# Kernel optimization log

Hardware: AMD Instinct MI355X
Metric: run time of the kernel (lower is better)

## Reference

```python
import jax, jax.numpy as jnp
import numpy as np

D_MODEL = 1024
NUM_HEADS = 16
HEAD_DIM = D_MODEL // NUM_HEADS
ALPHA = 1.0


def setup_inputs() -> dict:
    key = jax.random.key(0)
    ks = jax.random.split(key, 9)
    B, T, D = 2, 2048, D_MODEL
    s = 1.0 / np.sqrt(D)
    inp = {
        "x": jax.random.normal(ks[0], (B, T, D), dtype=jnp.float32),
        "Wq": jax.random.uniform(ks[1], (D, D), jnp.float32, -s, s),
        "bq": jax.random.uniform(ks[2], (D,), jnp.float32, -s, s),
        "Wk": jax.random.uniform(ks[3], (D, D), jnp.float32, -s, s),
        "bk": jax.random.uniform(ks[4], (D,), jnp.float32, -s, s),
        "Wv": jax.random.uniform(ks[5], (D, D), jnp.float32, -s, s),
        "bv": jax.random.uniform(ks[6], (D,), jnp.float32, -s, s),
        "Wo": jax.random.uniform(ks[7], (D, D), jnp.float32, -s, s),
        "bo": jax.random.uniform(ks[8], (D,), jnp.float32, -s, s),
    }
    return inp


def reference(x, Wq, bq, Wk, bk, Wv, bv, Wo, bo):
    B, T, D = x.shape
    H, hd = NUM_HEADS, HEAD_DIM

    def split_heads(y):  # [B,T,D] -> [B,H,T,hd]
        return y.reshape(B, T, H, hd).transpose(0, 2, 1, 3)

    Q = split_heads(x @ Wq.T + bq)
    K = split_heads(x @ Wk.T + bk)
    V = split_heads(x @ Wv.T + bv)

    scores = jnp.einsum('bhid,bhjd->bhij', Q, K) / jnp.sqrt(jnp.float32(hd))

    t = jnp.arange(T)
    delta = t[:, None] - t[None, :]  # [T,T], i - j
    causal_mask = delta < 0          # j > i (strict upper triangle)
    # similarity_power_law decay bias: -(delta)^alpha for delta >= 0, else 0
    decay = jnp.where(causal_mask, 0.0, -(delta.astype(jnp.float32) ** ALPHA))

    scores = jnp.where(causal_mask, -jnp.inf, scores) + decay
    attn = jax.nn.softmax(scores, axis=-1)

    out = jnp.einsum('bhij,bhjd->bhid', attn, V)
    out = out.transpose(0, 2, 1, 3).reshape(B, T, D)
    return out @ Wo.T + bo
```

## Files before the change

### kernel.cpp

```cpp
#include <hip/hip_runtime.h>

#define TT 2048
#define DD 1024
#define HH 16
#define HD 64
#define NTOK 4096
#define BK 32

typedef __bf16 bf16x8 __attribute__((ext_vector_type(8)));
typedef short short4v __attribute__((ext_vector_type(4)));
typedef float f32x4 __attribute__((ext_vector_type(4)));

__device__ __forceinline__ unsigned short f2bf(float f) {
  unsigned u = __float_as_uint(f);
  u += 0x7fffu + ((u >> 16) & 1u);
  return (unsigned short)(u >> 16);
}

#if __has_builtin(__builtin_amdgcn_mfma_f32_16x16x16bf16_1k)
__device__ __forceinline__ f32x4 mfma16(short4v a, short4v b, f32x4 c) {
  return __builtin_amdgcn_mfma_f32_16x16x16bf16_1k(a, b, c, 0, 0, 0);
}
#else
__device__ __forceinline__ f32x4 mfma16(short4v a, short4v b, f32x4 c) {
  asm("v_mfma_f32_16x16x16_bf16 %0, %1, %2, %0\n\ts_nop 7\n\ts_nop 7"
      : "+v"(c) : "v"(a), "v"(b));
  return c;
}
#endif

typedef void __attribute__((address_space(1))) as1_void;
typedef void __attribute__((address_space(3))) as3_void;
__device__ __forceinline__ void gl_lds16(const void* g, void* l) {
  __builtin_amdgcn_global_load_lds((as1_void*)g, (as3_void*)l, 16, 0, 0);
}

__global__ __launch_bounds__(256)
void wcmha_cast_all(const float4* __restrict__ x,  const float4* __restrict__ wq,
                    const float4* __restrict__ wk, const float4* __restrict__ wv,
                    const float4* __restrict__ wo,
                    ushort4* __restrict__ xb,  ushort4* __restrict__ wqb,
                    ushort4* __restrict__ wkb, ushort4* __restrict__ wvb,
                    ushort4* __restrict__ wob) {
  const int i = blockIdx.x * 256 + threadIdx.x;
  const float4* src;
  ushort4* dst;
  int off;
  if (i < 1048576) {
    src = x; dst = xb; off = i;
  } else {
    int j = i - 1048576;
    int sel = j >> 18;
    off = j & 262143;
    const float4* ws_[4] = {wq, wk, wv, wo};
    ushort4* wd_[4] = {wqb, wkb, wvb, wob};
    src = ws_[sel]; dst = wd_[sel];
  }
  float4 v = src[off];
  ushort4 o;
  o.x = f2bf(v.x); o.y = f2bf(v.y); o.z = f2bf(v.z); o.w = f2bf(v.w);
  dst[off] = o;
}

template <bool SWAP>
__device__ __forceinline__ void gemm128_core(
    const unsigned short* __restrict__ X, const unsigned short* __restrict__ W,
    int m0, int n0, unsigned short* As, unsigned short* Bs, f32x4 acc[4][4]) {
  const int tid = threadIdx.x;
  const int wid = tid >> 6, lane = tid & 63;
  const int m = lane & 15, quad = lane >> 4;
  const int wm = (wid >> 1) * 64, wn = (wid & 1) * 64;

  const int c0 = wid * 64 + lane;
  const int c1 = c0 + 256;
  const unsigned short* ga0 = X + (size_t)(m0 + (c0 >> 2)) * DD + (c0 & 3) * 8;
  const unsigned short* ga1 = X + (size_t)(m0 + (c1 >> 2)) * DD + (c1 & 3) * 8;
  const unsigned short* gb0 = W + (size_t)(n0 + (c0 >> 2)) * DD + (c0 & 3) * 8;
  const unsigned short* gb1 = W + (size_t)(n0 + (c1 >> 2)) * DD + (c1 & 3) * 8;
  unsigned short* la0 = As + wid * 512;
  unsigned short* la1 = As + 2048 + wid * 512;
  unsigned short* lb0 = Bs + wid * 512;
  unsigned short* lb1 = Bs + 2048 + wid * 512;

#pragma unroll
  for (int i = 0; i < 4; ++i)
#pragma unroll
    for (int j = 0; j < 4; ++j) acc[i][j] = (f32x4){0.f, 0.f, 0.f, 0.f};

  for (int k0 = 0; k0 < DD; k0 += BK) {
    gl_lds16(ga0 + k0, la0);
    gl_lds16(ga1 + k0, la1);
    gl_lds16(gb0 + k0, lb0);
    gl_lds16(gb1 + k0, lb1);
    __syncthreads();
    bf16x8 af[4], bf[4];
#pragma unroll
    for (int mi = 0; mi < 4; ++mi)
      af[mi] = *(const bf16x8*)&As[(wm + mi * 16 + m) * BK + quad * 8];
#pragma unroll
    for (int ni = 0; ni < 4; ++ni)
      bf[ni] = *(const bf16x8*)&Bs[(wn + ni * 16 + m) * BK + quad * 8];
#pragma unroll
    for (int mi = 0; mi < 4; ++mi)
#pragma unroll
      for (int ni = 0; ni < 4; ++ni)
        acc[mi][ni] = SWAP
            ? __builtin_amdgcn_mfma_f32_16x16x32_bf16(bf[ni], af[mi], acc[mi][ni], 0, 0, 0)
            : __builtin_amdgcn_mfma_f32_16x16x32_bf16(af[mi], bf[ni], acc[mi][ni], 0, 0, 0);
    __syncthreads();
  }
}

__global__ __launch_bounds__(256)
void wcmha_gemm_qkv(const unsigned short* __restrict__ X,
                    const unsigned short* __restrict__ Wq,
                    const unsigned short* __restrict__ Wk,
                    const unsigned short* __restrict__ Wv,
                    const float* __restrict__ bq, const float* __restrict__ bk,
                    const float* __restrict__ bv,
                    unsigned short* __restrict__ Qb,
                    unsigned short* __restrict__ Kb,
                    unsigned short* __restrict__ Vt) {
  __shared__ unsigned short As[128 * BK];
  __shared__ unsigned short Bs[128 * BK];
  const int mat = blockIdx.y >> 3;
  const int m0 = blockIdx.x * 128;
  const int n0 = (blockIdx.y & 7) * 128;

  const int lane = threadIdx.x & 63, wid = threadIdx.x >> 6;
  const int m = lane & 15, quad = lane >> 4;
  const int wm = (wid >> 1) * 64, wn = (wid & 1) * 64;

  f32x4 acc[4][4];
  if (mat < 2) {
    const unsigned short* W = mat ? Wk : Wq;
    const float* bias = mat ? bk : bq;
    unsigned short* dst = mat ? Kb : Qb;
    gemm128_core<false>(X, W, m0, n0, As, Bs, acc);
#pragma unroll
    for (int mi = 0; mi < 4; ++mi)
#pragma unroll
      for (int ni = 0; ni < 4; ++ni) {
        int col = n0 + wn + ni * 16 + m;
        int h = col >> 6, d = col & 63;
        float bb = bias[col];
#pragma unroll
        for (int r = 0; r < 4; ++r) {
          int row = m0 + wm + mi * 16 + quad * 4 + r;
          int b = row >> 11, t = row & (TT - 1);
          dst[((size_t)(b * HH + h) * TT + t) * HD + d] = f2bf(acc[mi][ni][r] + bb);
        }
      }
  } else {
    gemm128_core<true>(X, Wv, m0, n0, As, Bs, acc);
#pragma unroll
    for (int mi = 0; mi < 4; ++mi) {
      int row = m0 + wm + mi * 16 + m;
      int b = row >> 11, t = row & (TT - 1);
#pragma unroll
      for (int ni = 0; ni < 4; ++ni)
#pragma unroll
        for (int r = 0; r < 4; ++r) {
          int col = n0 + wn + ni * 16 + quad * 4 + r;
          int h = col >> 6, d = col & 63;
          Vt[((size_t)(b * HH + h) * HD + d) * TT + t] = f2bf(acc[mi][ni][r] + bv[col]);
        }
    }
  }
}

__global__ __launch_bounds__(256)
void wcmha_gemm_out(const unsigned short* __restrict__ X,
                    const unsigned short* __restrict__ W,
                    const float* __restrict__ bias,
                    float* __restrict__ Y) {
  __shared__ unsigned short As[128 * BK];
  __shared__ unsigned short Bs[64 * BK];
  const int tid = threadIdx.x;
  const int wid = tid >> 6, lane = tid & 63;
  const int m = lane & 15, quad = lane >> 4;
  const int m0 = blockIdx.x * 128;
  const int n0 = blockIdx.y * 64;
  const int wm = (wid >> 1) * 64, wn = (wid & 1) * 32;

  const int ca0 = wid * 128 + lane;
  const int ca1 = ca0 + 64;
  const int cb  = wid * 64 + lane;
  const unsigned short* aga = X + (size_t)(m0 + (ca0 >> 2)) * DD + (ca0 & 3) * 8;
  const unsigned short* agb = X + (size_t)(m0 + (ca1 >> 2)) * DD + (ca1 & 3) * 8;
  const unsigned short* bga = W + (size_t)(n0 + (cb >> 2)) * DD + (cb & 3) * 8;
  unsigned short* lda = &As[wid * 1024];
  unsigned short* ldb = &As[wid * 1024 + 512];
  unsigned short* ldc = &Bs[wid * 512];

  f32x4 acc[4][2];
#pragma unroll
  for (int i = 0; i < 4; ++i)
#pragma unroll
    for (int j = 0; j < 2; ++j) acc[i][j] = (f32x4){0.f, 0.f, 0.f, 0.f};

  for (int k0 = 0; k0 < DD; k0 += BK) {
    gl_lds16(aga + k0, lda);
    gl_lds16(agb + k0, ldb);
    gl_lds16(bga + k0, ldc);
    __syncthreads();
    bf16x8 af[4], bf[2];
#pragma unroll
    for (int mi = 0; mi < 4; ++mi)
      af[mi] = *(const bf16x8*)&As[(wm + mi * 16 + m) * BK + quad * 8];
#pragma unroll
    for (int ni = 0; ni < 2; ++ni)
      bf[ni] = *(const bf16x8*)&Bs[(wn + ni * 16 + m) * BK + quad * 8];
#pragma unroll
    for (int mi = 0; mi < 4; ++mi)
#pragma unroll
      for (int ni = 0; ni < 2; ++ni)
        acc[mi][ni] = __builtin_amdgcn_mfma_f32_16x16x32_bf16(af[mi], bf[ni], acc[mi][ni], 0, 0, 0);
    __syncthreads();
  }

#pragma unroll
  for (int mi = 0; mi < 4; ++mi)
#pragma unroll
    for (int ni = 0; ni < 2; ++ni) {
      int col = n0 + wn + ni * 16 + m;
      float bb = bias[col];
#pragma unroll
      for (int r = 0; r < 4; ++r) {
        int row = m0 + wm + mi * 16 + quad * 4 + r;
        Y[(size_t)row * DD + col] = acc[mi][ni][r] + bb;
      }
    }
}

__global__ __launch_bounds__(256)
void wcmha_attn(const unsigned short* __restrict__ Qb,
                const unsigned short* __restrict__ Kb,
                const unsigned short* __restrict__ Vt,
                unsigned short* __restrict__ O) {
  const int wid = threadIdx.x >> 6, lane = threadIdx.x & 63;
  const int gw = (blockIdx.x << 2) + wid;
  const int qt = gw & 127, bh = gw >> 7;
  const int qbase = qt << 4;
  const int il = lane & 15, quad = lane >> 4;
  const int ig = qbase + il;

  const unsigned short* q_ptr = Qb + (size_t)bh * TT * HD;
  const unsigned short* k_ptr = Kb + (size_t)bh * TT * HD;
  const unsigned short* v_ptr = Vt + (size_t)bh * HD * TT;

  const bf16x8 qf0 = *(const bf16x8*)(q_ptr + (size_t)ig * HD + quad * 8);
  const bf16x8 qf1 = *(const bf16x8*)(q_ptr + (size_t)ig * HD + 32 + quad * 8);

  const int j0 = (qbase >= 48) ? qbase - 48 : 0;

  f32x4 st[4];
#pragma unroll
  for (int jt = 0; jt < 4; ++jt) {
    const unsigned short* kp = k_ptr + (size_t)(j0 + jt * 16 + il) * HD;
    bf16x8 k0 = *(const bf16x8*)(kp + quad * 8);
    bf16x8 k1 = *(const bf16x8*)(kp + 32 + quad * 8);
    f32x4 a = {0.f, 0.f, 0.f, 0.f};
    a = __builtin_amdgcn_mfma_f32_16x16x32_bf16(k0, qf0, a, 0, 0, 0);
    a = __builtin_amdgcn_mfma_f32_16x16x32_bf16(k1, qf1, a, 0, 0, 0);
    st[jt] = a;
  }

  float mloc = -3.0e38f;
#pragma unroll
  for (int jt = 0; jt < 4; ++jt)
#pragma unroll
    for (int r = 0; r < 4; ++r) {
      int jg = j0 + jt * 16 + quad * 4 + r;
      float v = (jg > ig) ? -3.0e38f : st[jt][r] * 0.125f - (float)(ig - jg);
      st[jt][r] = v;
      mloc = fmaxf(mloc, v);
    }
  mloc = fmaxf(mloc, __shfl_xor(mloc, 16));
  mloc = fmaxf(mloc, __shfl_xor(mloc, 32));

  float rs = 0.f;
  short4v pf[4];
#pragma unroll
  for (int jt = 0; jt < 4; ++jt)
#pragma unroll
    for (int r = 0; r < 4; ++r) {
      float p = __expf(st[jt][r] - mloc);
      rs += p;
      pf[jt][r] = (short)f2bf(p);
    }
  rs += __shfl_xor(rs, 16);
  rs += __shfl_xor(rs, 32);

  f32x4 o_acc[4];
#pragma unroll
  for (int nt = 0; nt < 4; ++nt) o_acc[nt] = (f32x4){0.f, 0.f, 0.f, 0.f};
#pragma unroll
  for (int jt = 0; jt < 4; ++jt)
#pragma unroll
    for (int nt = 0; nt < 4; ++nt) {
      short4v vf = *(const short4v*)(v_ptr + (size_t)(nt * 16 + il) * TT +
                                     j0 + jt * 16 + quad * 4);
      o_acc[nt] = mfma16(vf, pf[jt], o_acc[nt]);
    }

  const float inv_l = 1.f / rs;
  const int b = bh >> 4, hh = bh & 15;
  unsigned short* ob = O + ((size_t)(b * TT + ig)) * DD + hh * HD;
#pragma unroll
  for (int nt = 0; nt < 4; ++nt)
#pragma unroll
    for (int r = 0; r < 4; ++r)
      ob[nt * 16 + quad * 4 + r] = f2bf(o_acc[nt][r] * inv_l);
}

extern "C" void kernel_launch(void* const* d_in, const int* in_sizes, int n_in,
                              void* d_out, int out_size, void* d_ws, size_t ws_size,
                              hipStream_t stream) {
  const float* x  = (const float*)d_in[0];
  const float* Wq = (const float*)d_in[1];
  const float* bq = (const float*)d_in[2];
  const float* Wk = (const float*)d_in[3];
  const float* bk = (const float*)d_in[4];
  const float* Wv = (const float*)d_in[5];
  const float* bv = (const float*)d_in[6];
  const float* Wo = (const float*)d_in[7];
  const float* bo = (const float*)d_in[8];

  char* ws = (char*)d_ws;
  unsigned short* xb  = (unsigned short*)(ws);
  unsigned short* wqb = (unsigned short*)(ws + (8u << 20));
  unsigned short* wkb = wqb + (1u << 20);
  unsigned short* wvb = wkb + (1u << 20);
  unsigned short* wob = wvb + (1u << 20);
  unsigned short* Qb  = (unsigned short*)(ws + (16u << 20));
  unsigned short* Kb  = (unsigned short*)(ws + (24u << 20));
  unsigned short* Vt  = (unsigned short*)(ws + (32u << 20));
  unsigned short* Ob  = xb;

  wcmha_cast_all<<<8192, 256, 0, stream>>>(
      (const float4*)x, (const float4*)Wq, (const float4*)Wk,
      (const float4*)Wv, (const float4*)Wo,
      (ushort4*)xb, (ushort4*)wqb, (ushort4*)wkb, (ushort4*)wvb, (ushort4*)wob);

  wcmha_gemm_qkv<<<dim3(32, 24), 256, 0, stream>>>(xb, wqb, wkb, wvb,
                                                   bq, bk, bv, Qb, Kb, Vt);

  wcmha_attn<<<1024, 256, 0, stream>>>(Qb, Kb, Vt, Ob);

  wcmha_gemm_out<<<dim3(32, 16), 256, 0, stream>>>(Ob, wob, bo, (float*)d_out);
}
```

Baseline: 170.0 us.

## Double-buffer GEMM LDS tiles with XOR swizzle and unify QKV/out GEMM core

Replaces the single-buffered GEMM main loop with a double-buffered one. The next K tile's global-to-LDS loads are issued before the current tile is computed, and one barrier per iteration replaces two. Each row's 16-byte chunk index is XOR-swizzled on both the load and the read side to reduce LDS bank conflicts. Both the QKV and output projection kernels now share a templated core, at the cost of twice the LDS per block, which may lower occupancy.

```diff
diff --git a/kernel.cpp b/kernel.cpp
--- a/kernel.cpp
+++ b/kernel.cpp
@@ -5,7 +5,6 @@
 #define HH 16
 #define HD 64
 #define NTOK 4096
-#define BK 32
 
 typedef __bf16 bf16x8 __attribute__((ext_vector_type(8)));
 typedef short short4v __attribute__((ext_vector_type(4)));
@@ -62,52 +61,79 @@
   dst[off] = o;
 }
 
-template <bool SWAP>
-__device__ __forceinline__ void gemm128_core(
-    const unsigned short* __restrict__ X, const unsigned short* __restrict__ W,
-    int m0, int n0, unsigned short* As, unsigned short* Bs, f32x4 acc[4][4]) {
-  const int tid = threadIdx.x;
-  const int wid = tid >> 6, lane = tid & 63;
+template <int BN_, bool SWAP>
+__device__ __forceinline__ void gemm_db(const unsigned short* __restrict__ X,
+                                        const unsigned short* __restrict__ W,
+                                        int m0, int n0,
+                                        unsigned short* As, unsigned short* Bs,
+                                        f32x4 acc[4][BN_ / 32]) {
+  constexpr int NI = BN_ / 32;
+  constexpr int JB = (BN_ * 4) / 256;
+  const int tid = threadIdx.x, wid = tid >> 6, lane = tid & 63;
   const int m = lane & 15, quad = lane >> 4;
-  const int wm = (wid >> 1) * 64, wn = (wid & 1) * 64;
-
-  const int c0 = wid * 64 + lane;
-  const int c1 = c0 + 256;
-  const unsigned short* ga0 = X + (size_t)(m0 + (c0 >> 2)) * DD + (c0 & 3) * 8;
-  const unsigned short* ga1 = X + (size_t)(m0 + (c1 >> 2)) * DD + (c1 & 3) * 8;
-  const unsigned short* gb0 = W + (size_t)(n0 + (c0 >> 2)) * DD + (c0 & 3) * 8;
-  const unsigned short* gb1 = W + (size_t)(n0 + (c1 >> 2)) * DD + (c1 & 3) * 8;
-  unsigned short* la0 = As + wid * 512;
-  unsigned short* la1 = As + 2048 + wid * 512;
-  unsigned short* lb0 = Bs + wid * 512;
-  unsigned short* lb1 = Bs + 2048 + wid * 512;
+  const int wm = (wid >> 1) * 64, wn = (wid & 1) * (BN_ / 2);
+  const int xq = (quad ^ ((m >> 1) & 3)) * 8;
+
+  const unsigned short* gA[2];
+  const unsigned short* gB[JB];
+#pragma unroll
+  for (int j = 0; j < 2; ++j) {
+    int c = wid * 64 + lane + j * 256;
+    gA[j] = X + (size_t)(m0 + (c >> 2)) * DD + ((c & 3) ^ ((c >> 3) & 3)) * 8;
+  }
+#pragma unroll
+  for (int j = 0; j < JB; ++j) {
+    int c = wid * 64 + lane + j * 256;
+    gB[j] = W + (size_t)(n0 + (c >> 2)) * DD + ((c & 3) ^ ((c >> 3) & 3)) * 8;
+  }
+  unsigned short* lA[2][2];
+  unsigned short* lB[2][JB];
+#pragma unroll
+  for (int p = 0; p < 2; ++p) {
+#pragma unroll
+    for (int j = 0; j < 2; ++j)
+      lA[p][j] = As + p * (128 * 32) + (wid * 64 + j * 256) * 8;
+#pragma unroll
+    for (int j = 0; j < JB; ++j)
+      lB[p][j] = Bs + p * (BN_ * 32) + (wid * 64 + j * 256) * 8;
+  }
 
 #pragma unroll
   for (int i = 0; i < 4; ++i)
 #pragma unroll
-    for (int j = 0; j < 4; ++j) acc[i][j] = (f32x4){0.f, 0.f, 0.f, 0.f};
-
-  for (int k0 = 0; k0 < DD; k0 += BK) {
-    gl_lds16(ga0 + k0, la0);
-    gl_lds16(ga1 + k0, la1);
-    gl_lds16(gb0 + k0, lb0);
-    gl_lds16(gb1 + k0, lb1);
+    for (int j = 0; j < NI; ++j) acc[i][j] = (f32x4){0.f, 0.f, 0.f, 0.f};
+
+#pragma unroll
+  for (int j = 0; j < 2; ++j) gl_lds16(gA[j], lA[0][j]);
+#pragma unroll
+  for (int j = 0; j < JB; ++j) gl_lds16(gB[j], lB[0][j]);
+
+  for (int k = 0; k < 32; ++k) {
+    const int p = k & 1;
     __syncthreads();
-    bf16x8 af[4], bf[4];
+    if (k < 31) {
+      const int k1 = (k + 1) * 32;
+#pragma unroll
+      for (int j = 0; j < 2; ++j) gl_lds16(gA[j] + k1, lA[p ^ 1][j]);
+#pragma unroll
+      for (int j = 0; j < JB; ++j) gl_lds16(gB[j] + k1, lB[p ^ 1][j]);
+    }
+    const unsigned short* ap = As + p * (128 * 32);
+    const unsigned short* bp = Bs + p * (BN_ * 32);
+    bf16x8 af[4], bf[NI];
 #pragma unroll
     for (int mi = 0; mi < 4; ++mi)
-      af[mi] = *(const bf16x8*)&As[(wm + mi * 16 + m) * BK + quad * 8];
-#pragma unroll
-    for (int ni = 0; ni < 4; ++ni)
-      bf[ni] = *(const bf16x8*)&Bs[(wn + ni * 16 + m) * BK + quad * 8];
+      af[mi] = *(const bf16x8*)&ap[(wm + mi * 16 + m) * 32 + xq];
+#pragma unroll
+    for (int ni = 0; ni < NI; ++ni)
+      bf[ni] = *(const bf16x8*)&bp[(wn + ni * 16 + m) * 32 + xq];
 #pragma unroll
     for (int mi = 0; mi < 4; ++mi)
 #pragma unroll
-      for (int ni = 0; ni < 4; ++ni)
+      for (int ni = 0; ni < NI; ++ni)
         acc[mi][ni] = SWAP
             ? __builtin_amdgcn_mfma_f32_16x16x32_bf16(bf[ni], af[mi], acc[mi][ni], 0, 0, 0)
             : __builtin_amdgcn_mfma_f32_16x16x32_bf16(af[mi], bf[ni], acc[mi][ni], 0, 0, 0);
-    __syncthreads();
   }
 }
 
@@ -121,8 +147,8 @@
                     unsigned short* __restrict__ Qb,
                     unsigned short* __restrict__ Kb,
                     unsigned short* __restrict__ Vt) {
-  __shared__ unsigned short As[128 * BK];
-  __shared__ unsigned short Bs[128 * BK];
+  __shared__ unsigned short As[2 * 128 * 32];
+  __shared__ unsigned short Bs[2 * 128 * 32];
   const int mat = blockIdx.y >> 3;
   const int m0 = blockIdx.x * 128;
   const int n0 = (blockIdx.y & 7) * 128;
@@ -136,7 +162,7 @@
     const unsigned short* W = mat ? Wk : Wq;
     const float* bias = mat ? bk : bq;
     unsigned short* dst = mat ? Kb : Qb;
-    gemm128_core<false>(X, W, m0, n0, As, Bs, acc);
+    gemm_db<128, false>(X, W, m0, n0, As, Bs, acc);
 #pragma unroll
     for (int mi = 0; mi < 4; ++mi)
 #pragma unroll
@@ -152,7 +178,7 @@
         }
       }
   } else {
-    gemm128_core<true>(X, Wv, m0, n0, As, Bs, acc);
+    gemm_db<128, true>(X, Wv, m0, n0, As, Bs, acc);
 #pragma unroll
     for (int mi = 0; mi < 4; ++mi) {
       int row = m0 + wm + mi * 16 + m;
@@ -174,50 +200,16 @@
                     const unsigned short* __restrict__ W,
                     const float* __restrict__ bias,
                     float* __restrict__ Y) {
-  __shared__ unsigned short As[128 * BK];
-  __shared__ unsigned short Bs[64 * BK];
-  const int tid = threadIdx.x;
-  const int wid = tid >> 6, lane = tid & 63;
-  const int m = lane & 15, quad = lane >> 4;
+  __shared__ unsigned short As[2 * 128 * 32];
+  __shared__ unsigned short Bs[2 * 64 * 32];
   const int m0 = blockIdx.x * 128;
   const int n0 = blockIdx.y * 64;
+  const int lane = threadIdx.x & 63, wid = threadIdx.x >> 6;
+  const int m = lane & 15, quad = lane >> 4;
   const int wm = (wid >> 1) * 64, wn = (wid & 1) * 32;
 
-  const int ca0 = wid * 128 + lane;
-  const int ca1 = ca0 + 64;
-  const int cb  = wid * 64 + lane;
-  const unsigned short* aga = X + (size_t)(m0 + (ca0 >> 2)) * DD + (ca0 & 3) * 8;
-  const unsigned short* agb = X + (size_t)(m0 + (ca1 >> 2)) * DD + (ca1 & 3) * 8;
-  const unsigned short* bga = W + (size_t)(n0 + (cb >> 2)) * DD + (cb & 3) * 8;
-  unsigned short* lda = &As[wid * 1024];
-  unsigned short* ldb = &As[wid * 1024 + 512];
-  unsigned short* ldc = &Bs[wid * 512];
-
   f32x4 acc[4][2];
-#pragma unroll
-  for (int i = 0; i < 4; ++i)
-#pragma unroll
-    for (int j = 0; j < 2; ++j) acc[i][j] = (f32x4){0.f, 0.f, 0.f, 0.f};
-
-  for (int k0 = 0; k0 < DD; k0 += BK) {
-    gl_lds16(aga + k0, lda);
-    gl_lds16(agb + k0, ldb);
-    gl_lds16(bga + k0, ldc);
-    __syncthreads();
-    bf16x8 af[4], bf[2];
-#pragma unroll
-    for (int mi = 0; mi < 4; ++mi)
-      af[mi] = *(const bf16x8*)&As[(wm + mi * 16 + m) * BK + quad * 8];
-#pragma unroll
-    for (int ni = 0; ni < 2; ++ni)
-      bf[ni] = *(const bf16x8*)&Bs[(wn + ni * 16 + m) * BK + quad * 8];
-#pragma unroll
-    for (int mi = 0; mi < 4; ++mi)
-#pragma unroll
-      for (int ni = 0; ni < 2; ++ni)
-        acc[mi][ni] = __builtin_amdgcn_mfma_f32_16x16x32_bf16(af[mi], bf[ni], acc[mi][ni], 0, 0, 0);
-    __syncthreads();
-  }
+  gemm_db<64, false>(X, W, m0, n0, As, Bs, acc);
 
 #pragma unroll
   for (int mi = 0; mi < 4; ++mi)
```

Result: no change. 167.8 us (-1.3%).
